# Kernel tuning notes

Hardware: AMD Instinct MI355X
Metric: run time of the kernel (lower is better)

## Reference

```python
import jax, jax.numpy as jnp
import numpy as np

FACTOR = 2
KERNEL_SIZE = 3
GAIN = 1


def _setup_kernel(k):
    k = np.asarray(k, dtype=np.float32)
    if k.ndim == 1:
        k = np.outer(k, k)
    k /= k.sum()
    return k


def _fir_kernel():
    # k = _setup_kernel([1,3,1]) * (gain * factor**2), shape [1,1,3,3]
    k = _setup_kernel([1, 3, 1]) * (GAIN * FACTOR ** 2)
    return jnp.asarray(k)[None, None]


def setup_inputs() -> dict:
    key = jax.random.key(0)
    k1, k2 = jax.random.split(key)
    x = jax.random.normal(k1, (16, 512, 64, 64), dtype=jnp.float32)
    w = jax.random.normal(k2, (256, 512, 3, 3), dtype=jnp.float32) * 0.05
    return {"x": x, "w": w}


def reference(x, w):
    fir = _fir_kernel()  # [1,1,3,3]
    # source uses self.k.shape[0] == 1 (unsqueezed leading dim) in the pad formula
    p = 1 - FACTOR + KERNEL_SIZE - 1          # = 1
    pad0 = (p + 1) // 2 + FACTOR - 1          # = 2
    pad1 = p // 2                              # = 0

    inC, outC, kh, kw = w.shape
    w = w.reshape(outC, inC, kh, kw)          # pure reshape (data reinterpretation), as in source

    # F.conv_transpose2d(x, w, stride=factor) == conv with lhs_dilation, flipped kernel,
    # in/out channel dims swapped, full padding (kh-1).
    w_conv = jnp.flip(w, axis=(2, 3)).transpose(1, 0, 2, 3)  # OIHW [inC, outC, kh, kw]
    x = jax.lax.conv_general_dilated(
        x, w_conv, window_strides=(1, 1),
        padding=((kh - 1, kh - 1), (kw - 1, kw - 1)),
        lhs_dilation=(FACTOR, FACTOR),
        dimension_numbers=('NCHW', 'OIHW', 'NCHW'))
    N, C, H, W = x.shape  # H = 2*H_in + 1 (odd)

    # zero-interleave block is a no-op: local factor == 1 when self.factor == 2
    x = jnp.pad(x, ((0, 0), (0, 0), (pad0, pad1), (pad0, pad1)))
    # depthwise FIR: fold channels into batch, conv with single-channel 3x3 filter
    x = x.reshape(N * C, 1, H + pad0 + pad1, W + pad0 + pad1)
    x = jax.lax.conv_general_dilated(
        x, fir, window_strides=(1, 1), padding='VALID',
        dimension_numbers=('NCHW', 'OIHW', 'NCHW'))
    x = x.reshape(N, C, H, W)

    if W % 2 != 0:  # static shape check, matches source's odd-size crop
        x = x[:, :, :W - 1, :W - 1]
    return x
```

## Files before the change

kernel.cpp:

```cpp
#include <hip/hip_runtime.h>
#include <hip/hip_bf16.h>


typedef __attribute__((ext_vector_type(8))) short short8;
typedef __attribute__((ext_vector_type(4))) float float4v;

#define XP_ELEMS ((size_t)16 * 65 * 65 * 512)
#define WP_ELEMS ((size_t)9 * 256 * 512)
#define YP_ELEMS ((size_t)4 * 16 * 256 * 4096)

__device__ __forceinline__ void gl_lds16(const __hip_bfloat16* g, __hip_bfloat16* l) {
    __builtin_amdgcn_global_load_lds(
        (const __attribute__((address_space(1))) void*)g,
        (__attribute__((address_space(3))) void*)l, 16, 0, 0);
}

__global__ __launch_bounds__(256) void prep_kernel(
    const float* __restrict__ w, __hip_bfloat16* __restrict__ wp,
    __hip_bfloat16* __restrict__ xp) {
    int idx = blockIdx.x * 256 + (int)threadIdx.x;
    {
        int c  = idx & 511;
        int o  = (idx >> 9) & 255;
        int ab = idx >> 17;
        int a = ab / 3, b = ab % 3;
        wp[idx] = __float2bfloat16(w[((size_t)(c * 256 + o) * 3 + a) * 3 + b]);
    }
    if (idx < 16 * 65 * 512) {
        int c = idx & 511;
        int t = (idx >> 9) % 65;
        int n = idx / (65 * 512);
        __hip_bfloat16 z = __float2bfloat16(0.f);
        xp[(((size_t)(n * 65) + 0) * 65 + t) * 512 + c] = z;
        xp[(((size_t)(n * 65) + t) * 65 + 0) * 512 + c] = z;
    }
}

__global__ __launch_bounds__(256) void pack_x_kernel(
    const float* __restrict__ x, __hip_bfloat16* __restrict__ xp) {
    int i = blockIdx.x;
    int n = blockIdx.y;
    int tid = (int)threadIdx.x;
    __shared__ float tile[64][65];
    const int j4 = (tid & 15) * 4;
    for (int c0 = 0; c0 < 512; c0 += 64) {
        __syncthreads();
#pragma unroll
        for (int rr = 0; rr < 4; rr++) {
            int cl = rr * 16 + (tid >> 4);
            float4v v = *(const float4v*)(
                x + (((size_t)(n * 512 + c0 + cl) * 64) + i) * 64 + j4);
#pragma unroll
            for (int t = 0; t < 4; t++) tile[cl][j4 + t] = v[t];
        }
        __syncthreads();
#pragma unroll
        for (int pass = 0; pass < 2; pass++) {
            int task = pass * 256 + tid;
            int j  = task >> 3;
            int cg = task & 7;
            union { short8 v; unsigned short h[8]; } u;
#pragma unroll
            for (int r = 0; r < 8; r++) {
                __hip_bfloat16 b = __float2bfloat16(tile[cg * 8 + r][j]);
                u.h[r] = *(unsigned short*)&b;
            }
            *(short8*)(xp + (((size_t)(n * 65) + i + 1) * 65 + (j + 1)) * 512 +
                       c0 + cg * 8) = u.v;
        }
    }
}

__global__ __launch_bounds__(256) void mfma_conv_kernel(
    const __hip_bfloat16* __restrict__ xp, const __hip_bfloat16* __restrict__ wp,
    __hip_bfloat16* __restrict__ yp) {
    const int flat = (int)blockIdx.x;
    const int nf   = ((flat & 7) << 9) + (flat >> 3);
    const int p    = nf & 3;
    const int o0   = ((nf >> 2) & 1) * 128;
    const int mt   = nf >> 3;
    const int ph = p >> 1, pw = p & 1;
    const int n  = mt >> 5;
    const int i0 = (mt & 31) << 1;
    const int tid  = (int)threadIdx.x;
    const int wave = tid >> 6, lane = tid & 63;
    const int wm = wave & 1, wn = wave >> 1;
    const int lrow = lane & 15, quad = lane >> 4;
    const int m0j   = wave * 16 + (lane >> 2);
    const int klane = (lane & 3) * 8;

    __shared__ __align__(16) __hip_bfloat16 lA[128 * 32];
    __shared__ __align__(16) __hip_bfloat16 lB[128 * 32];

    float4v acc[4][4];
#pragma unroll
    for (int fm = 0; fm < 4; fm++)
#pragma unroll
        for (int fn = 0; fn < 4; fn++) acc[fm][fn] = (float4v)0.f;

    __hip_bfloat16* la0 = lA + wave * 512;
    __hip_bfloat16* la1 = lA + 2048 + wave * 512;
    __hip_bfloat16* lb0 = lB + wave * 512;
    __hip_bfloat16* lb1 = lB + 2048 + wave * 512;

    const int nrt = ph ? 1 : 2, nct = pw ? 1 : 2;
    for (int rt = 0; rt < nrt; rt++) {
        const int drp = ph ? 1 : rt;
        const int a   = ph ? 1 : (rt ? 0 : 2);
        for (int ct = 0; ct < nct; ct++) {
            const int dsp = pw ? 1 : ct;
            const int b   = pw ? 1 : (ct ? 0 : 2);
            const int ab  = a * 3 + b;
            const __hip_bfloat16* A0 =
                xp + (((size_t)(n * 65 + i0 + drp)) * 65 + m0j + dsp) * 512 + klane;
            const __hip_bfloat16* A1 = A0 + (size_t)65 * 512;
            const __hip_bfloat16* B0 =
                wp + ((size_t)(ab * 256 + o0 + m0j)) * 512 + klane;
            const __hip_bfloat16* B1 = B0 + (size_t)64 * 512;

            for (int c0 = 0; c0 < 512; c0 += 32) {
                __syncthreads();
                gl_lds16(A0 + c0, la0);
                gl_lds16(A1 + c0, la1);
                gl_lds16(B0 + c0, lb0);
                gl_lds16(B1 + c0, lb1);
                __syncthreads();
                short8 af[4], bv[4];
#pragma unroll
                for (int fm = 0; fm < 4; fm++)
                    af[fm] = *(const short8*)(lA + ((wm * 64 + fm * 16 + lrow) * 32 + quad * 8));
#pragma unroll
                for (int fn = 0; fn < 4; fn++)
                    bv[fn] = *(const short8*)(lB + ((wn * 64 + fn * 16 + lrow) * 32 + quad * 8));
#pragma unroll
                for (int fm = 0; fm < 4; fm++)
#pragma unroll
                    for (int fn = 0; fn < 4; fn++)
                        acc[fm][fn] = __builtin_amdgcn_mfma_f32_16x16x32_bf16(
                            af[fm], bv[fn], acc[fm][fn], 0, 0, 0);
            }
        }
    }

#pragma unroll
    for (int fm = 0; fm < 4; fm++) {
        int j0 = fm * 16 + quad * 4;
#pragma unroll
        for (int fn = 0; fn < 4; fn++) {
            int o = o0 + wn * 64 + fn * 16 + lrow;
            union { ushort4 v; __hip_bfloat16 h[4]; } u;
#pragma unroll
            for (int r = 0; r < 4; r++) u.h[r] = __float2bfloat16(acc[fm][fn][r]);
            *(ushort4*)(yp + (((size_t)(p * 4096 + n * 256 + o)) << 12) +
                        ((i0 + wm) << 6) + j0) = u.v;
        }
    }
}

__device__ __forceinline__ float bf_lo(unsigned u) { return __uint_as_float(u << 16); }
__device__ __forceinline__ float bf_hi(unsigned u) { return __uint_as_float(u & 0xffff0000u); }

__global__ __launch_bounds__(256) void fir_kernel(
    const __hip_bfloat16* __restrict__ yp, float* __restrict__ out) {
    const int no  = blockIdx.x;
    const int tid = (int)threadIdx.x;

    __shared__ __align__(16) unsigned short ylds[4 * 64 * 64];

    const unsigned short* ysrc = (const unsigned short*)yp;
#pragma unroll
    for (int k = 0; k < 8; k++) {
        int chunk = k * 256 + tid;
        int q   = chunk >> 9;
        int off = (chunk & 511) << 3;
        *(short8*)(ylds + q * 4096 + off) =
            *(const short8*)(ysrc + (((size_t)(q * 4096 + no)) << 12) + off);
    }
    __syncthreads();

    const unsigned* yw = (const unsigned*)ylds;

    const int qp = tid & 31;
    const int iw = tid >> 5;

    const float rw[2][2][2] = {{{0.4f, 0.4f}, {1.2f, 0.f}},
                               {{0.f, 1.2f}, {0.4f, 0.4f}}};

    for (int s = 0; s < 8; s++) {
        const int I = s * 8 + iw;

        float Y3[2][2][2][3];
#pragma unroll
        for (int q = 0; q < 4; q++) {
            int phh = q >> 1, pww = q & 1;
#pragma unroll
            for (int k = 0; k < 2; k++) {
                int ih = I - 1 + k;
                float c0 = 0.f, c1 = 0.f, c2 = 0.f;
                if (ih >= 0) {
                    const unsigned* row = yw + (q * 64 + ih) * 32;
                    unsigned wb = row[qp];
                    c1 = bf_lo(wb);
                    c2 = bf_hi(wb);
                    if (qp > 0) c0 = bf_hi(row[qp - 1]);
                }
                Y3[phh][pww][k][0] = c0;
                Y3[phh][pww][k][1] = c1;
                Y3[phh][pww][k][2] = c2;
            }
        }

        float res[2][4];
#pragma unroll
        for (int t = 0; t < 2; t++) {
            float cs[2][2][2];
#pragma unroll
            for (int phh = 0; phh < 2; phh++)
#pragma unroll
                for (int k = 0; k < 2; k++)
#pragma unroll
                    for (int ew = 0; ew < 2; ew++) {
                        float sv = 0.f;
#pragma unroll
                        for (int pww = 0; pww < 2; pww++)
#pragma unroll
                            for (int l = 0; l < 2; l++)
                                sv += rw[ew][pww][l] * Y3[phh][pww][k][t + l];
                        cs[phh][k][ew] = sv;
                    }
#pragma unroll
            for (int eh = 0; eh < 2; eh++)
#pragma unroll
                for (int ew = 0; ew < 2; ew++) {
                    float sv = 0.f;
#pragma unroll
                    for (int phh = 0; phh < 2; phh++)
#pragma unroll
                        for (int k = 0; k < 2; k++)
                            sv += rw[eh][phh][k] * cs[phh][k][ew];
                    res[eh][t * 2 + ew] = sv;
                }
        }

        size_t base = ((size_t)no << 14) + ((size_t)(2 * I) << 7) + 4 * qp;
        float4v v0 = {res[0][0], res[0][1], res[0][2], res[0][3]};
        float4v v1 = {res[1][0], res[1][1], res[1][2], res[1][3]};
        *(float4v*)(out + base)       = v0;
        *(float4v*)(out + base + 128) = v1;
    }
}

__global__ __launch_bounds__(256) void fused_direct_kernel(
    const float* __restrict__ x, const float* __restrict__ w,
    float* __restrict__ out) {
    int idx = blockIdx.x * 256 + (int)threadIdx.x;
    int w_ = idx & 127, h = (idx >> 7) & 127, no = idx >> 14;
    int o = no & 255, n = no >> 8;
    int I = h >> 1, J = w_ >> 1;
    const float fr0 = 0.4f, fr1 = 1.2f, fr2 = 0.4f;
    float gh[3][3]; int rh[3]; int nh;
    if ((h & 1) == 0) {
        nh = 3;
        rh[0] = I - 2; gh[0][0] = 0.f; gh[0][1] = 0.f; gh[0][2] = fr0;
        rh[1] = I - 1; gh[1][0] = fr0; gh[1][1] = fr1; gh[1][2] = fr2;
        rh[2] = I;     gh[2][0] = fr2; gh[2][1] = 0.f; gh[2][2] = 0.f;
    } else {
        nh = 2;
        rh[0] = I - 1; gh[0][0] = 0.f; gh[0][1] = fr0; gh[0][2] = fr1;
        rh[1] = I;     gh[1][0] = fr1; gh[1][1] = fr2; gh[1][2] = 0.f;
    }
    float gw[3][3]; int cw[3]; int nw;
    if ((w_ & 1) == 0) {
        nw = 3;
        cw[0] = J - 2; gw[0][0] = 0.f; gw[0][1] = 0.f; gw[0][2] = fr0;
        cw[1] = J - 1; gw[1][0] = fr0; gw[1][1] = fr1; gw[1][2] = fr2;
        cw[2] = J;     gw[2][0] = fr2; gw[2][1] = 0.f; gw[2][2] = 0.f;
    } else {
        nw = 2;
        cw[0] = J - 1; gw[0][0] = 0.f; gw[0][1] = fr0; gw[0][2] = fr1;
        cw[1] = J;     gw[1][0] = fr1; gw[1][1] = fr2; gw[1][2] = 0.f;
    }
    float acc = 0.f;
    for (int c = 0; c < 512; c++) {
        const float* xb = x + ((size_t)(n * 512 + c) << 12);
        const float* wb = w + (size_t)(c * 256 + o) * 9;
        float tmp[3][3];
#pragma unroll
        for (int dr = 0; dr < 3; dr++) tmp[dr][0] = tmp[dr][1] = tmp[dr][2] = 0.f;
        for (int dr = 0; dr < nh; dr++) {
            int r = rh[dr]; if (r < 0) continue;
            for (int ds = 0; ds < nw; ds++) {
                int s = cw[ds]; if (s < 0) continue;
                float xv = xb[(r << 6) + s];
                tmp[dr][0] += gw[ds][0] * xv;
                tmp[dr][1] += gw[ds][1] * xv;
                tmp[dr][2] += gw[ds][2] * xv;
            }
        }
#pragma unroll
        for (int a = 0; a < 3; a++) {
            float xg0 = 0.f, xg1 = 0.f, xg2 = 0.f;
            for (int dr = 0; dr < nh; dr++) {
                float g = gh[dr][a];
                xg0 += g * tmp[dr][0]; xg1 += g * tmp[dr][1]; xg2 += g * tmp[dr][2];
            }
            acc += xg0 * wb[a * 3] + xg1 * wb[a * 3 + 1] + xg2 * wb[a * 3 + 2];
        }
    }
    out[idx] = acc;
}

extern "C" void kernel_launch(void* const* d_in, const int* in_sizes, int n_in,
                              void* d_out, int out_size, void* d_ws, size_t ws_size,
                              hipStream_t stream)
{
    (void)in_sizes; (void)n_in; (void)out_size;
    const float* x = (const float*)d_in[0];
    const float* w = (const float*)d_in[1];
    float* out = (float*)d_out;

    const size_t need = (XP_ELEMS + WP_ELEMS + YP_ELEMS) * sizeof(__hip_bfloat16);
    if (ws_size >= need) {
        __hip_bfloat16* xp = (__hip_bfloat16*)d_ws;
        __hip_bfloat16* wp = xp + XP_ELEMS;
        __hip_bfloat16* yp = wp + WP_ELEMS;
        prep_kernel<<<dim3((int)(WP_ELEMS / 256)), dim3(256), 0, stream>>>(w, wp, xp);
        pack_x_kernel<<<dim3(64, 16), dim3(256), 0, stream>>>(x, xp);
        mfma_conv_kernel<<<dim3(4096), dim3(256), 0, stream>>>(xp, wp, yp);
        fir_kernel<<<dim3(4096), dim3(256), 0, stream>>>(yp, out);
    } else {
        fused_direct_kernel<<<dim3((int)(YP_ELEMS / 256)), dim3(256), 0, stream>>>(x, w, out);
    }
}
```

Measured before the change: 679.2 us.

## Double-buffer LDS tiles in MFMA conv and flatten tap loop with 3D grid

Replaces the single-buffered LDS staging with a double buffer, so the next K-slice's global-to-LDS loads are issued before the current slice's MFMAs. This cuts one of the two barriers per step. The nested tap/channel loops become a single flat step loop with precomputed per-tap pointers. The block-index swizzle is replaced by a plain 3D grid (o-tile, m-tile, phase), which changes block scheduling order and L2 locality. Doubling LDS to 32KB may reduce occupancy.

```diff
diff --git a/kernel.cpp b/kernel.cpp
--- a/kernel.cpp
+++ b/kernel.cpp
@@ -74,12 +74,9 @@
 __global__ __launch_bounds__(256) void mfma_conv_kernel(
     const __hip_bfloat16* __restrict__ xp, const __hip_bfloat16* __restrict__ wp,
     __hip_bfloat16* __restrict__ yp) {
-    const int flat = (int)blockIdx.x;
-    const int nf   = ((flat & 7) << 9) + (flat >> 3);
-    const int p    = nf & 3;
-    const int o0   = ((nf >> 2) & 1) * 128;
-    const int mt   = nf >> 3;
-    const int ph = p >> 1, pw = p & 1;
+    const int p  = blockIdx.z, ph = p >> 1, pw = p & 1;
+    const int o0 = blockIdx.x * 128;
+    const int mt = blockIdx.y;
     const int n  = mt >> 5;
     const int i0 = (mt & 31) << 1;
     const int tid  = (int)threadIdx.x;
@@ -89,8 +86,7 @@
     const int m0j   = wave * 16 + (lane >> 2);
     const int klane = (lane & 3) * 8;
 
-    __shared__ __align__(16) __hip_bfloat16 lA[128 * 32];
-    __shared__ __align__(16) __hip_bfloat16 lB[128 * 32];
+    __shared__ __align__(16) __hip_bfloat16 lds[2 * 8192];
 
     float4v acc[4][4];
 #pragma unroll
@@ -98,48 +94,69 @@
 #pragma unroll
         for (int fn = 0; fn < 4; fn++) acc[fm][fn] = (float4v)0.f;
 
-    __hip_bfloat16* la0 = lA + wave * 512;
-    __hip_bfloat16* la1 = lA + 2048 + wave * 512;
-    __hip_bfloat16* lb0 = lB + wave * 512;
-    __hip_bfloat16* lb1 = lB + 2048 + wave * 512;
-
     const int nrt = ph ? 1 : 2, nct = pw ? 1 : 2;
-    for (int rt = 0; rt < nrt; rt++) {
-        const int drp = ph ? 1 : rt;
-        const int a   = ph ? 1 : (rt ? 0 : 2);
-        for (int ct = 0; ct < nct; ct++) {
-            const int dsp = pw ? 1 : ct;
-            const int b   = pw ? 1 : (ct ? 0 : 2);
-            const int ab  = a * 3 + b;
-            const __hip_bfloat16* A0 =
-                xp + (((size_t)(n * 65 + i0 + drp)) * 65 + m0j + dsp) * 512 + klane;
-            const __hip_bfloat16* A1 = A0 + (size_t)65 * 512;
-            const __hip_bfloat16* B0 =
-                wp + ((size_t)(ab * 256 + o0 + m0j)) * 512 + klane;
-            const __hip_bfloat16* B1 = B0 + (size_t)64 * 512;
-
-            for (int c0 = 0; c0 < 512; c0 += 32) {
-                __syncthreads();
-                gl_lds16(A0 + c0, la0);
-                gl_lds16(A1 + c0, la1);
-                gl_lds16(B0 + c0, lb0);
-                gl_lds16(B1 + c0, lb1);
-                __syncthreads();
-                short8 af[4], bv[4];
-#pragma unroll
-                for (int fm = 0; fm < 4; fm++)
-                    af[fm] = *(const short8*)(lA + ((wm * 64 + fm * 16 + lrow) * 32 + quad * 8));
-#pragma unroll
-                for (int fn = 0; fn < 4; fn++)
-                    bv[fn] = *(const short8*)(lB + ((wn * 64 + fn * 16 + lrow) * 32 + quad * 8));
-#pragma unroll
-                for (int fm = 0; fm < 4; fm++)
-#pragma unroll
-                    for (int fn = 0; fn < 4; fn++)
-                        acc[fm][fn] = __builtin_amdgcn_mfma_f32_16x16x32_bf16(
-                            af[fm], bv[fn], acc[fm][fn], 0, 0, 0);
-            }
-        }
+    const int nt  = nrt * nct;
+
+    auto mkA = [&](int tap) -> const __hip_bfloat16* {
+        int rt = (nct == 2) ? (tap >> 1) : tap;
+        int ct = (nct == 2) ? (tap & 1) : 0;
+        int drp = ph ? 1 : rt;
+        int dsp = pw ? 1 : ct;
+        return xp + (((size_t)(n * 65 + i0 + drp)) * 65 + m0j + dsp) * 512 + klane;
+    };
+    auto mkB = [&](int tap) -> const __hip_bfloat16* {
+        int rt = (nct == 2) ? (tap >> 1) : tap;
+        int ct = (nct == 2) ? (tap & 1) : 0;
+        int a = ph ? 1 : (rt ? 0 : 2);
+        int b = pw ? 1 : (ct ? 0 : 2);
+        return wp + ((size_t)((a * 3 + b) * 256 + o0 + m0j)) * 512 + klane;
+    };
+    const __hip_bfloat16* A0p = mkA(0); const __hip_bfloat16* B0p = mkB(0);
+    const __hip_bfloat16* A1p = mkA(1); const __hip_bfloat16* B1p = mkB(1);
+    const __hip_bfloat16* A2p = mkA(2); const __hip_bfloat16* B2p = mkB(2);
+    const __hip_bfloat16* A3p = mkA(3); const __hip_bfloat16* B3p = mkB(3);
+
+    const int nsteps = nt << 4;
+
+    {
+        __hip_bfloat16* dst = lds;
+        gl_lds16(A0p,                     dst + wave * 512);
+        gl_lds16(A0p + (size_t)65 * 512,  dst + 2048 + wave * 512);
+        gl_lds16(B0p,                     dst + 4096 + wave * 512);
+        gl_lds16(B0p + (size_t)64 * 512,  dst + 6144 + wave * 512);
+    }
+    __syncthreads();
+
+    for (int t = 0; t < nsteps; t++) {
+        const int cb = t & 1;
+        if (t + 1 < nsteps) {
+            const int tap = (t + 1) >> 4;
+            const int c0  = ((t + 1) & 15) << 5;
+            const __hip_bfloat16* At =
+                (tap == 0) ? A0p : (tap == 1) ? A1p : (tap == 2) ? A2p : A3p;
+            const __hip_bfloat16* Bt =
+                (tap == 0) ? B0p : (tap == 1) ? B1p : (tap == 2) ? B2p : B3p;
+            __hip_bfloat16* dst = lds + (cb ^ 1) * 8192;
+            gl_lds16(At + c0,                    dst + wave * 512);
+            gl_lds16(At + c0 + (size_t)65 * 512, dst + 2048 + wave * 512);
+            gl_lds16(Bt + c0,                    dst + 4096 + wave * 512);
+            gl_lds16(Bt + c0 + (size_t)64 * 512, dst + 6144 + wave * 512);
+        }
+        const __hip_bfloat16* src = lds + cb * 8192;
+        short8 af[4], bv[4];
+#pragma unroll
+        for (int fm = 0; fm < 4; fm++)
+            af[fm] = *(const short8*)(src + ((wm * 64 + fm * 16 + lrow) * 32 + quad * 8));
+#pragma unroll
+        for (int fn = 0; fn < 4; fn++)
+            bv[fn] = *(const short8*)(src + 4096 + ((wn * 64 + fn * 16 + lrow) * 32 + quad * 8));
+#pragma unroll
+        for (int fm = 0; fm < 4; fm++)
+#pragma unroll
+            for (int fn = 0; fn < 4; fn++)
+                acc[fm][fn] = __builtin_amdgcn_mfma_f32_16x16x32_bf16(
+                    af[fm], bv[fn], acc[fm][fn], 0, 0, 0);
+        __syncthreads();
     }
 
 #pragma unroll
@@ -326,7 +343,7 @@
         __hip_bfloat16* yp = wp + WP_ELEMS;
         prep_kernel<<<dim3((int)(WP_ELEMS / 256)), dim3(256), 0, stream>>>(w, wp, xp);
         pack_x_kernel<<<dim3(64, 16), dim3(256), 0, stream>>>(x, xp);
-        mfma_conv_kernel<<<dim3(4096), dim3(256), 0, stream>>>(xp, wp, yp);
+        mfma_conv_kernel<<<dim3(2, 512, 4), dim3(256), 0, stream>>>(xp, wp, yp);
         fir_kernel<<<dim3(4096), dim3(256), 0, stream>>>(yp, out);
     } else {
         fused_direct_kernel<<<dim3((int)(YP_ELEMS / 256)), dim3(256), 0, stream>>>(x, w, out);
```

Result: faster. 620.3 us (-8.7%).

## Load shared input halo once per channel chunk and compute all taps from LDS

Applied to the files above, without the earlier changes.

The conv kernel no longer loops over the 1-4 transposed-conv taps with separate global loads of input rows. For each 32-channel chunk it now loads a 3-row-by-65-column input halo once, plus the weights for every tap, then runs each tap's MFMAs from shifted LDS offsets. This removes repeated A-tile fetches and the per-tap barrier pairs. It also replaces the swizzled 1D grid with a plain 3D grid and requests 3 blocks per SM. In exchange LDS use per block grows, and the loss of the block swizzle may change cache locality.

```diff
diff --git a/kernel.cpp b/kernel.cpp
--- a/kernel.cpp
+++ b/kernel.cpp
@@ -71,15 +71,12 @@
     }
 }
 
-__global__ __launch_bounds__(256) void mfma_conv_kernel(
+__global__ __launch_bounds__(256, 3) void mfma_conv_kernel(
     const __hip_bfloat16* __restrict__ xp, const __hip_bfloat16* __restrict__ wp,
     __hip_bfloat16* __restrict__ yp) {
-    const int flat = (int)blockIdx.x;
-    const int nf   = ((flat & 7) << 9) + (flat >> 3);
-    const int p    = nf & 3;
-    const int o0   = ((nf >> 2) & 1) * 128;
-    const int mt   = nf >> 3;
-    const int ph = p >> 1, pw = p & 1;
+    const int p  = blockIdx.z, ph = p >> 1, pw = p & 1;
+    const int o0 = blockIdx.x * 128;
+    const int mt = blockIdx.y;
     const int n  = mt >> 5;
     const int i0 = (mt & 31) << 1;
     const int tid  = (int)threadIdx.x;
@@ -89,8 +86,8 @@
     const int m0j   = wave * 16 + (lane >> 2);
     const int klane = (lane & 3) * 8;
 
-    __shared__ __align__(16) __hip_bfloat16 lA[128 * 32];
-    __shared__ __align__(16) __hip_bfloat16 lB[128 * 32];
+    __shared__ __align__(16) __hip_bfloat16 lA[256 * 32];
+    __shared__ __align__(16) __hip_bfloat16 lB[4 * 128 * 32];
 
     float4v acc[4][4];
 #pragma unroll
@@ -98,47 +95,75 @@
 #pragma unroll
         for (int fn = 0; fn < 4; fn++) acc[fm][fn] = (float4v)0.f;
 
-    __hip_bfloat16* la0 = lA + wave * 512;
-    __hip_bfloat16* la1 = lA + 2048 + wave * 512;
-    __hip_bfloat16* lb0 = lB + wave * 512;
-    __hip_bfloat16* lb1 = lB + 2048 + wave * 512;
-
-    const int nrt = ph ? 1 : 2, nct = pw ? 1 : 2;
-    for (int rt = 0; rt < nrt; rt++) {
-        const int drp = ph ? 1 : rt;
-        const int a   = ph ? 1 : (rt ? 0 : 2);
-        for (int ct = 0; ct < nct; ct++) {
-            const int dsp = pw ? 1 : ct;
-            const int b   = pw ? 1 : (ct ? 0 : 2);
-            const int ab  = a * 3 + b;
-            const __hip_bfloat16* A0 =
-                xp + (((size_t)(n * 65 + i0 + drp)) * 65 + m0j + dsp) * 512 + klane;
-            const __hip_bfloat16* A1 = A0 + (size_t)65 * 512;
-            const __hip_bfloat16* B0 =
-                wp + ((size_t)(ab * 256 + o0 + m0j)) * 512 + klane;
-            const __hip_bfloat16* B1 = B0 + (size_t)64 * 512;
-
-            for (int c0 = 0; c0 < 512; c0 += 32) {
-                __syncthreads();
-                gl_lds16(A0 + c0, la0);
-                gl_lds16(A1 + c0, la1);
-                gl_lds16(B0 + c0, lb0);
-                gl_lds16(B1 + c0, lb1);
-                __syncthreads();
-                short8 af[4], bv[4];
-#pragma unroll
-                for (int fm = 0; fm < 4; fm++)
-                    af[fm] = *(const short8*)(lA + ((wm * 64 + fm * 16 + lrow) * 32 + quad * 8));
-#pragma unroll
-                for (int fn = 0; fn < 4; fn++)
-                    bv[fn] = *(const short8*)(lB + ((wn * 64 + fn * 16 + lrow) * 32 + quad * 8));
-#pragma unroll
-                for (int fm = 0; fm < 4; fm++)
-#pragma unroll
-                    for (int fn = 0; fn < 4; fn++)
-                        acc[fm][fn] = __builtin_amdgcn_mfma_f32_16x16x32_bf16(
-                            af[fm], bv[fn], acc[fm][fn], 0, 0, 0);
-            }
+    const int nct = pw ? 1 : 2;
+    const int nt  = (ph ? 1 : 2) * nct;
+
+    const __hip_bfloat16* bA = xp + (size_t)n * 65 * 65 * 512;
+    const int Rb = (wave << 4) + (lane >> 2);
+    int offA0, offA1, offA2, offA3;
+    {
+        int R0 = Rb, R1 = Rb + 64, R2 = Rb + 128, R3 = Rb + 192;
+        if (R3 > 194) R3 = 194;
+        offA0 = ((i0 + R0 / 65) * 65 + R0 % 65) * 512 + klane;
+        offA1 = ((i0 + R1 / 65) * 65 + R1 % 65) * 512 + klane;
+        offA2 = ((i0 + R2 / 65) * 65 + R2 % 65) * 512 + klane;
+        offA3 = ((i0 + R3 / 65) * 65 + R3 % 65) * 512 + klane;
+    }
+    const __hip_bfloat16* bB = wp + (size_t)(o0 + m0j) * 512 + klane;
+
+    const int rt1 = (nct == 2) ? 0 : 1, ct1 = (nct == 2) ? 1 : 0;
+    const int aoffL = lrow * 32 + quad * 8;
+    const int aoff0 = ((ph ? 1 : 0)   + wm) * 2080 + (pw ? 1 : 0)   * 32 + aoffL;
+    const int aoff1 = ((ph ? 1 : rt1) + wm) * 2080 + (pw ? 1 : ct1) * 32 + aoffL;
+    const int aoff2 = ((ph ? 1 : 1)   + wm) * 2080 + (pw ? 1 : 0)   * 32 + aoffL;
+    const int aoff3 = ((ph ? 1 : 1)   + wm) * 2080 + (pw ? 1 : 1)   * 32 + aoffL;
+    const int ab0 = ((ph ? 1 : 2) * 3 + (pw ? 1 : 2)) * 131072;
+    const int ab1 = ((ph ? 1 : (rt1 ? 0 : 2)) * 3 + (pw ? 1 : (ct1 ? 0 : 2))) * 131072;
+    const int ab2 = ((ph ? 1 : 0) * 3 + (pw ? 1 : 2)) * 131072;
+    const int ab3 = ((ph ? 1 : 0) * 3 + (pw ? 1 : 0)) * 131072;
+
+    const int boff = (wn * 64 + lrow) * 32 + quad * 8;
+
+    auto compute_tap = [&](int aoffT, const __hip_bfloat16* lBt) {
+        short8 af[4], bv[4];
+#pragma unroll
+        for (int fm = 0; fm < 4; fm++)
+            af[fm] = *(const short8*)(lA + aoffT + fm * 512);
+#pragma unroll
+        for (int fn = 0; fn < 4; fn++)
+            bv[fn] = *(const short8*)(lBt + boff + fn * 512);
+#pragma unroll
+        for (int fm = 0; fm < 4; fm++)
+#pragma unroll
+            for (int fn = 0; fn < 4; fn++)
+                acc[fm][fn] = __builtin_amdgcn_mfma_f32_16x16x32_bf16(
+                    af[fm], bv[fn], acc[fm][fn], 0, 0, 0);
+    };
+
+    for (int c0 = 0; c0 < 512; c0 += 32) {
+        __syncthreads();
+        gl_lds16(bA + offA0 + c0, lA +        wave * 512);
+        gl_lds16(bA + offA1 + c0, lA + 2048 + wave * 512);
+        gl_lds16(bA + offA2 + c0, lA + 4096 + wave * 512);
+        gl_lds16(bA + offA3 + c0, lA + 6144 + wave * 512);
+        gl_lds16(bB + (ab0 + c0),         lB +        wave * 512);
+        gl_lds16(bB + (ab0 + 32768 + c0), lB + 2048 + wave * 512);
+        if (nt > 1) {
+            gl_lds16(bB + (ab1 + c0),         lB + 4096 + wave * 512);
+            gl_lds16(bB + (ab1 + 32768 + c0), lB + 6144 + wave * 512);
+        }
+        if (nt > 2) {
+            gl_lds16(bB + (ab2 + c0),         lB + 8192  + wave * 512);
+            gl_lds16(bB + (ab2 + 32768 + c0), lB + 10240 + wave * 512);
+            gl_lds16(bB + (ab3 + c0),         lB + 12288 + wave * 512);
+            gl_lds16(bB + (ab3 + 32768 + c0), lB + 14336 + wave * 512);
+        }
+        __syncthreads();
+        compute_tap(aoff0, lB);
+        if (nt > 1) compute_tap(aoff1, lB + 4096);
+        if (nt > 2) {
+            compute_tap(aoff2, lB + 8192);
+            compute_tap(aoff3, lB + 12288);
         }
     }
 
@@ -326,7 +351,7 @@
         __hip_bfloat16* yp = wp + WP_ELEMS;
         prep_kernel<<<dim3((int)(WP_ELEMS / 256)), dim3(256), 0, stream>>>(w, wp, xp);
         pack_x_kernel<<<dim3(64, 16), dim3(256), 0, stream>>>(x, xp);
-        mfma_conv_kernel<<<dim3(4096), dim3(256), 0, stream>>>(xp, wp, yp);
+        mfma_conv_kernel<<<dim3(2, 512, 4), dim3(256), 0, stream>>>(xp, wp, yp);
         fir_kernel<<<dim3(4096), dim3(256), 0, stream>>>(yp, out);
     } else {
         fused_direct_kernel<<<dim3((int)(YP_ELEMS / 256)), dim3(256), 0, stream>>>(x, w, out);
```

Measured after the change: 594.4 us. 12.5% less time.
